# Performance work log

Measured on AMD Instinct MI355X. Metric: run time of the kernel, lower is better.

## Reference

```python
import jax, jax.numpy as jnp
import numpy as np

E = 1024
H = 16
D = E // H
S = 2048
B = 2

def setup_inputs() -> dict:
    key = jax.random.key(0)
    ks = jax.random.split(key, 5)
    x = jax.random.normal(ks[0], (B, S, E), dtype=jnp.float32)
    W_qkv = jax.random.normal(ks[1], (E, 3 * E), dtype=jnp.float32) / np.sqrt(E)
    b_qkv = jax.random.normal(ks[2], (3 * E,), dtype=jnp.float32) * 0.02
    W_out = jax.random.normal(ks[3], (E, E), dtype=jnp.float32) / np.sqrt(E)
    b_out = jax.random.normal(ks[4], (E,), dtype=jnp.float32) * 0.02
    return {"x": x, "W_qkv": W_qkv, "b_qkv": b_qkv, "W_out": W_out, "b_out": b_out}

def reference(x, W_qkv, b_qkv, W_out, b_out):
    b, s, e = x.shape
    qkv = x @ W_qkv + b_qkv                      # [B,S,3E]
    q, k, v = jnp.split(qkv, 3, axis=-1)
    # [B,S,E] -> [B,H,S,D]
    q = q.reshape(b, s, H, D).transpose(0, 2, 1, 3)
    k = k.reshape(b, s, H, D).transpose(0, 2, 1, 3)
    v = v.reshape(b, s, H, D).transpose(0, 2, 1, 3)
    scale = 1.0 / np.sqrt(D)
    att = jnp.einsum('bhqd,bhkd->bhqk', q, k) * scale
    causal = jnp.tril(jnp.ones((s, s), dtype=bool))
    att = jnp.where(causal[None, None], att, -jnp.inf)
    att = jax.nn.softmax(att, axis=-1)
    out = jnp.einsum('bhqk,bhkd->bhqd', att, v)  # [B,H,S,D]
    out = out.transpose(0, 2, 1, 3).reshape(b, s, e)
    return out @ W_out + b_out
```

## Files before the change

kernel.cpp:

```cpp
#include <hip/hip_runtime.h>

typedef unsigned short u16;
typedef __bf16  bf16x8 __attribute__((ext_vector_type(8)));
typedef float   f32x4  __attribute__((ext_vector_type(4)));
typedef unsigned int   u32x4 __attribute__((ext_vector_type(4)));
typedef unsigned short u16x4 __attribute__((ext_vector_type(4)));
typedef unsigned short u16x8 __attribute__((ext_vector_type(8)));

#define BB 2
#define HH 16
#define DD 64
#define SS 2048
#define EE 1024

#define QSCALE 0.1803368801111244f

static __device__ __forceinline__ u16 f2bf(float f) {
    unsigned int u = __float_as_uint(f);
    u += 0x7FFFu + ((u >> 16) & 1u);
    return (u16)(u >> 16);
}

union BfCast { u32x4 u; bf16x8 b; };
static __device__ __forceinline__ bf16x8 ldb8(const u16* p) {
    BfCast x; x.u = *(const u32x4*)p; return x.b;
}

static __device__ __forceinline__ void gload16(const u16* g, u16* l) {
    __builtin_amdgcn_global_load_lds(
        (const __attribute__((address_space(1))) unsigned int*)g,
        (__attribute__((address_space(3))) unsigned int*)l, 16, 0, 0);
}

#define UG (32 * 512)
static __device__ __forceinline__ int kidx(int s, int d) {
    return (((s >> 4) * 2 + (d >> 5)) * 512) + ((((d >> 3) & 3) * 16 + (s & 15)) * 8) + (d & 7);
}
static __device__ __forceinline__ int vidx(int key, int d) {
    return (((key >> 5) * 4 + (d >> 4)) * 512) + ((((key >> 3) & 3) * 16 + (d & 15)) * 8) + (key & 7);
}

__global__ __launch_bounds__(256) void prep_kernel(
    const float* __restrict__ x,    u16* __restrict__ xb,
    const float* __restrict__ Wqkv, u16* __restrict__ wqkvT,
    const float* __restrict__ Wout, u16* __restrict__ woutT)
{
    __shared__ float tile[32][33];
    const int bid = blockIdx.x;
    if (bid < 2048) {
        const int t = bid * 256 + threadIdx.x;
        const int u = t >> 6, w = t & 63;
        const int m = (u >> 5) * 16 + (w & 15);
        const int k = (u & 31) * 32 + (w >> 4) * 8;
        const float* p = x + m * 1024 + k;
        const f32x4 a = *(const f32x4*)p;
        const f32x4 b = *(const f32x4*)(p + 4);
        u16x8 o;
        o[0] = f2bf(a[0]); o[1] = f2bf(a[1]); o[2] = f2bf(a[2]); o[3] = f2bf(a[3]);
        o[4] = f2bf(b[0]); o[5] = f2bf(b[1]); o[6] = f2bf(b[2]); o[7] = f2bf(b[3]);
        *(u16x8*)&xb[u * 512 + w * 8] = o;
        return;
    }
    const float* in; u16* out; int C, tb;
    if (bid < 2048 + 3072) { in = Wqkv; out = wqkvT; C = 3072; tb = bid - 2048; }
    else                   { in = Wout; out = woutT; C = 1024; tb = bid - 5120; }
    const int tx = threadIdx.x & 31;
    const int ty = threadIdx.x >> 5;
    const int ct = C >> 5;
    const int bc = tb % ct, br = tb / ct;
    const int c0 = bc * 32, r0 = br * 32;
    #pragma unroll
    for (int i = 0; i < 4; i++)
        tile[ty + i * 8][tx] = in[(r0 + ty + i * 8) * C + c0 + tx];
    __syncthreads();
    #pragma unroll
    for (int i = 0; i < 4; i++) {
        const int n = c0 + ty + i * 8;
        out[((n >> 4) * 32 + (r0 >> 5)) * 512 + (((tx >> 3) & 3) * 16 + (n & 15)) * 8 + (tx & 7)]
            = f2bf(tile[tx][ty + i * 8]);
    }
}

__global__ __launch_bounds__(256) void gemm_qkv_kernel(
    const u16* __restrict__ Af,
    const u16* __restrict__ Bf,
    const float* __restrict__ bias,
    u16* __restrict__ Qb, u16* __restrict__ Kb, u16* __restrict__ Vb)
{
    __shared__ __align__(16) u16 Us[2][12 * 512];
    const int lane = threadIdx.x & 63;
    const int wave = threadIdx.x >> 6;
    const int nb = 3 * EE / 128;
    const int tm = blockIdx.x / nb, tn = blockIdx.x % nb;
    const int lm = lane & 15, quad = lane >> 4;

    const u16* sp[3];
    #pragma unroll
    for (int j = 0; j < 3; j++) {
        const int idx = 3 * wave + j;
        sp[j] = (idx < 4) ? (Af + (tm * 4 + idx) * UG + lane * 8)
                          : (Bf + (tn * 8 + idx - 4) * UG + lane * 8);
    }
    u16* ld0 = &Us[0][3 * wave * 512];
    u16* ld1 = &Us[1][3 * wave * 512];

    const int wy = wave >> 1, wx = wave & 1;
    f32x4 acc[2][4] = {};

    gload16(sp[0], ld0);
    gload16(sp[1], ld0 + 512);
    gload16(sp[2], ld0 + 1024);

    for (int it = 0; it < 32; ++it) {
        const int cur = it & 1;
        __syncthreads();
        if (it + 1 < 32) {
            u16* ld = cur ? ld0 : ld1;
            const int ko = (it + 1) * 512;
            gload16(sp[0] + ko, ld);
            gload16(sp[1] + ko, ld + 512);
            gload16(sp[2] + ko, ld + 1024);
        }
        bf16x8 af[2], bf[4];
        #pragma unroll
        for (int i = 0; i < 2; i++)
            af[i] = ldb8(&Us[cur][(wy * 2 + i) * 512 + lane * 8]);
        #pragma unroll
        for (int i = 0; i < 4; i++)
            bf[i] = ldb8(&Us[cur][(4 + wx * 4 + i) * 512 + lane * 8]);
        #pragma unroll
        for (int mi = 0; mi < 2; mi++)
            #pragma unroll
            for (int ni = 0; ni < 4; ni++)
                acc[mi][ni] = __builtin_amdgcn_mfma_f32_16x16x32_bf16(af[mi], bf[ni], acc[mi][ni], 0, 0, 0);
    }

    const int gm0 = tm * 64 + wy * 32;
    const int gn0 = tn * 128 + wx * 64;
    #pragma unroll
    for (int ni = 0; ni < 4; ni++) {
        const int n = gn0 + ni * 16 + lm;
        const float bv = bias[n];
        const int which = n >> 10;
        const int e = n & 1023;
        const int h = e >> 6, d = e & 63;
        #pragma unroll
        for (int mi = 0; mi < 2; mi++) {
            if (which == 2) {
                const int m0 = gm0 + mi * 16 + quad * 4;
                const int b = m0 >> 11, key0 = m0 & 2047;
                u16x4 pk;
                #pragma unroll
                for (int r = 0; r < 4; r++) pk[r] = f2bf(acc[mi][ni][r] + bv);
                *(u16x4*)&Vb[(b * HH + h) * 131072 + vidx(key0, d)] = pk;
            } else if (which == 1) {
                #pragma unroll
                for (int r = 0; r < 4; r++) {
                    const int m = gm0 + mi * 16 + quad * 4 + r;
                    const int b = m >> 11, s = m & 2047;
                    Kb[(b * HH + h) * 131072 + kidx(s, d)] = f2bf(acc[mi][ni][r] + bv);
                }
            } else {
                #pragma unroll
                for (int r = 0; r < 4; r++) {
                    const int m = gm0 + mi * 16 + quad * 4 + r;
                    const int b = m >> 11, s = m & 2047;
                    Qb[((b * HH + h) * SS + s) * DD + d] = f2bf((acc[mi][ni][r] + bv) * QSCALE);
                }
            }
        }
    }
}

__global__ __launch_bounds__(256) void attn_kernel(
    const u16* __restrict__ Qb, const u16* __restrict__ Kb,
    const u16* __restrict__ Vb, u16* __restrict__ Ob)
{
    __shared__ __align__(16) u16 Ks[2][4096];
    __shared__ __align__(16) u16 Vs[2][4096];
    __shared__ __align__(16) u16 Plds[4 * 16 * 72];
    const int tid = threadIdx.x;
    const int lane = tid & 63, wave = tid >> 6;
    const int lm = lane & 15, quad = lane >> 4;
    const int bh = blockIdx.x & 31;
    const int qt = (SS / 64 - 1) - (blockIdx.x >> 5);
    const int q0 = qt * 64;
    const int qrow = q0 + wave * 16;
    const int b = bh >> 4, h = bh & 15;

    const u16* qbase = Qb + (bh * SS + qrow) * DD;
    const bf16x8 qf0 = ldb8(qbase + lm * DD + quad * 8);
    const bf16x8 qf1 = ldb8(qbase + lm * DD + 32 + quad * 8);

    const u16* ktile = Kb + bh * 131072;
    const u16* vtile = Vb + bh * 131072;
    u16* Pw = Plds + wave * (16 * 72);

    BfCast oc; oc.u = (u32x4){0x3F803F80u, 0x3F803F80u, 0x3F803F80u, 0x3F803F80u};
    const bf16x8 ones = oc.b;

    f32x4 oacc[4] = {};
    f32x4 lacc = {0.f, 0.f, 0.f, 0.f};

    const int ktmax = qt + 1;
    {
        const u16* kg = ktile + wave * 1024 + lane * 8;
        const u16* vg = vtile + wave * 1024 + lane * 8;
        gload16(kg,       &Ks[0][wave * 1024]);
        gload16(kg + 512, &Ks[0][wave * 1024 + 512]);
        gload16(vg,       &Vs[0][wave * 1024]);
        gload16(vg + 512, &Vs[0][wave * 1024 + 512]);
    }
    for (int kt = 0; kt < ktmax; ++kt) {
        const int cur = kt & 1;
        const int k0 = kt * 64;
        __syncthreads();
        if (kt + 1 < ktmax) {
            const u16* kg = ktile + (kt + 1) * 4096 + wave * 1024 + lane * 8;
            const u16* vg = vtile + (kt + 1) * 4096 + wave * 1024 + lane * 8;
            gload16(kg,       &Ks[cur ^ 1][wave * 1024]);
            gload16(kg + 512, &Ks[cur ^ 1][wave * 1024 + 512]);
            gload16(vg,       &Vs[cur ^ 1][wave * 1024]);
            gload16(vg + 512, &Vs[cur ^ 1][wave * 1024 + 512]);
        }

        f32x4 s[4];
        #pragma unroll
        for (int g = 0; g < 4; g++) {
            f32x4 z = {0.f, 0.f, 0.f, 0.f};
            z    = __builtin_amdgcn_mfma_f32_16x16x32_bf16(ldb8(&Ks[cur][(g * 2) * 512 + lane * 8]), qf0, z, 0, 0, 0);
            s[g] = __builtin_amdgcn_mfma_f32_16x16x32_bf16(ldb8(&Ks[cur][(g * 2 + 1) * 512 + lane * 8]), qf1, z, 0, 0, 0);
        }
        if (k0 + 63 > qrow) {
            const int lim = qrow + lm - k0 - quad * 4;
            #pragma unroll
            for (int g = 0; g < 4; g++)
                #pragma unroll
                for (int r = 0; r < 4; r++)
                    if (g * 16 + r > lim) s[g][r] = -INFINITY;
        }
        #pragma unroll
        for (int g = 0; g < 4; g++) {
            u16x4 pk;
            #pragma unroll
            for (int r = 0; r < 4; r++) pk[r] = f2bf(__builtin_amdgcn_exp2f(s[g][r]));
            *(u16x4*)&Pw[lm * 72 + g * 16 + quad * 4] = pk;
        }
        const bf16x8 pf0 = ldb8(&Pw[lm * 72 + quad * 8]);
        const bf16x8 pf1 = ldb8(&Pw[lm * 72 + 32 + quad * 8]);
        lacc = __builtin_amdgcn_mfma_f32_16x16x32_bf16(ones, pf0, lacc, 0, 0, 0);
        lacc = __builtin_amdgcn_mfma_f32_16x16x32_bf16(ones, pf1, lacc, 0, 0, 0);
        #pragma unroll
        for (int dg = 0; dg < 4; dg++) {
            oacc[dg] = __builtin_amdgcn_mfma_f32_16x16x32_bf16(ldb8(&Vs[cur][dg * 512 + lane * 8]), pf0, oacc[dg], 0, 0, 0);
            oacc[dg] = __builtin_amdgcn_mfma_f32_16x16x32_bf16(ldb8(&Vs[cur][(4 + dg) * 512 + lane * 8]), pf1, oacc[dg], 0, 0, 0);
        }
    }
    const float inv = 1.0f / lacc[0];
    u16* ob = Ob + (((b * SS + qrow) >> 4) * 32 + h * 2) * 512;
    #pragma unroll
    for (int dg = 0; dg < 4; dg++) {
        u16x4 pk;
        #pragma unroll
        for (int r = 0; r < 4; r++) pk[r] = f2bf(oacc[dg][r] * inv);
        *(u16x4*)&ob[(dg >> 1) * 512 + (((dg * 2 + (quad >> 1)) & 3) * 16 + lm) * 8 + (quad & 1) * 4] = pk;
    }
}

__global__ __launch_bounds__(256) void gemm_out_kernel(
    const u16* __restrict__ Af,
    const u16* __restrict__ Bf,
    const float* __restrict__ bias,
    float* __restrict__ Out)
{
    __shared__ __align__(16) u16 Us[2][8 * 512];
    const int lane = threadIdx.x & 63;
    const int wave = threadIdx.x >> 6;
    const int nb = EE / 64;
    const int tm = blockIdx.x / nb, tn = blockIdx.x % nb;
    const int lm = lane & 15, quad = lane >> 4;

    const u16* sp[2];
    #pragma unroll
    for (int j = 0; j < 2; j++) {
        const int idx = 2 * wave + j;
        sp[j] = (idx < 4) ? (Af + (tm * 4 + idx) * UG + lane * 8)
                          : (Bf + (tn * 4 + idx - 4) * UG + lane * 8);
    }
    u16* ld0 = &Us[0][2 * wave * 512];
    u16* ld1 = &Us[1][2 * wave * 512];

    const int wy = wave >> 1, wx = wave & 1;
    f32x4 acc[2][2] = {};

    gload16(sp[0], ld0);
    gload16(sp[1], ld0 + 512);

    for (int it = 0; it < 32; ++it) {
        const int cur = it & 1;
        __syncthreads();
        if (it + 1 < 32) {
            u16* ld = cur ? ld0 : ld1;
            const int ko = (it + 1) * 512;
            gload16(sp[0] + ko, ld);
            gload16(sp[1] + ko, ld + 512);
        }
        bf16x8 af[2], bf[2];
        #pragma unroll
        for (int i = 0; i < 2; i++) {
            af[i] = ldb8(&Us[cur][(wy * 2 + i) * 512 + lane * 8]);
            bf[i] = ldb8(&Us[cur][(4 + wx * 2 + i) * 512 + lane * 8]);
        }
        #pragma unroll
        for (int mi = 0; mi < 2; mi++)
            #pragma unroll
            for (int ni = 0; ni < 2; ni++)
                acc[mi][ni] = __builtin_amdgcn_mfma_f32_16x16x32_bf16(af[mi], bf[ni], acc[mi][ni], 0, 0, 0);
    }

    const int gm0 = tm * 64 + wy * 32;
    const int gn0 = tn * 64 + wx * 32;
    #pragma unroll
    for (int ni = 0; ni < 2; ni++) {
        const int n = gn0 + ni * 16 + lm;
        const float bv = bias[n];
        #pragma unroll
        for (int mi = 0; mi < 2; mi++)
            #pragma unroll
            for (int r = 0; r < 4; r++)
                Out[(gm0 + mi * 16 + quad * 4 + r) * EE + n] = acc[mi][ni][r] + bv;
    }
}

extern "C" void kernel_launch(void* const* d_in, const int* in_sizes, int n_in,
                              void* d_out, int out_size, void* d_ws, size_t ws_size,
                              hipStream_t stream)
{
    const float* x     = (const float*)d_in[0];
    const float* Wqkv  = (const float*)d_in[1];
    const float* bqkv  = (const float*)d_in[2];
    const float* Wout  = (const float*)d_in[3];
    const float* bout  = (const float*)d_in[4];
    float* out = (float*)d_out;

    char* ws = (char*)d_ws;
    u16* xb    = (u16*)(ws + 0);
    u16* wqkvT = (u16*)(ws + 8388608);
    u16* woutT = (u16*)(ws + 14680064);
    u16* Qb    = (u16*)(ws + 16777216);
    u16* Kb    = (u16*)(ws + 25165824);
    u16* Vb    = (u16*)(ws + 33554432);
    u16* Ob    = (u16*)(ws + 41943040);
    if (ws_size < 50331648) return;

    prep_kernel<<<2048 + 3072 + 1024, 256, 0, stream>>>(x, xb, Wqkv, wqkvT, Wout, woutT);
    gemm_qkv_kernel<<<(BB * SS / 64) * (3 * EE / 128), 256, 0, stream>>>(xb, wqkvT, bqkv, Qb, Kb, Vb);
    attn_kernel<<<BB * HH * (SS / 64), 256, 0, stream>>>(Qb, Kb, Vb, Ob);
    gemm_out_kernel<<<(BB * SS / 64) * (EE / 64), 256, 0, stream>>>(Ob, woutT, bout, out);
}
```

Measured before the change: 173.9 us.

## Enlarge GEMM tiles and load A fragments directly into registers

Both GEMMs now use larger output tiles: QKV goes from 64x128 to 128x128 and the output projection from 64x64 to 64x128. Only the shared B tile is staged in LDS, and each wave loads its A fragments straight from global memory into registers with software double buffering. The aim is more reuse per loaded byte, less LDS traffic and fewer blocks. In exchange there are more accumulator registers and fewer blocks in flight, so latency hiding may suffer.

```diff
diff --git a/kernel.cpp b/kernel.cpp
--- a/kernel.cpp
+++ b/kernel.cpp
@@ -81,61 +81,77 @@
     }
 }
 
-__global__ __launch_bounds__(256) void gemm_qkv_kernel(
+__global__ __launch_bounds__(256, 3) void gemm_qkv_kernel(
     const u16* __restrict__ Af,
     const u16* __restrict__ Bf,
     const float* __restrict__ bias,
     u16* __restrict__ Qb, u16* __restrict__ Kb, u16* __restrict__ Vb)
 {
-    __shared__ __align__(16) u16 Us[2][12 * 512];
+    __shared__ __align__(16) u16 Bs[2][8 * 512];
     const int lane = threadIdx.x & 63;
     const int wave = threadIdx.x >> 6;
     const int nb = 3 * EE / 128;
     const int tm = blockIdx.x / nb, tn = blockIdx.x % nb;
     const int lm = lane & 15, quad = lane >> 4;
-
-    const u16* sp[3];
-    #pragma unroll
-    for (int j = 0; j < 3; j++) {
-        const int idx = 3 * wave + j;
-        sp[j] = (idx < 4) ? (Af + (tm * 4 + idx) * UG + lane * 8)
-                          : (Bf + (tn * 8 + idx - 4) * UG + lane * 8);
-    }
-    u16* ld0 = &Us[0][3 * wave * 512];
-    u16* ld1 = &Us[1][3 * wave * 512];
-
     const int wy = wave >> 1, wx = wave & 1;
-    f32x4 acc[2][4] = {};
-
-    gload16(sp[0], ld0);
-    gload16(sp[1], ld0 + 512);
-    gload16(sp[2], ld0 + 1024);
-
-    for (int it = 0; it < 32; ++it) {
-        const int cur = it & 1;
+
+    const u16* bg = Bf + (tn * 8 + 2 * wave) * UG + lane * 8;
+    u16* bl0 = &Bs[0][2 * wave * 512];
+    u16* bl1 = &Bs[1][2 * wave * 512];
+    const u16* ag[4];
+    #pragma unroll
+    for (int i = 0; i < 4; i++)
+        ag[i] = Af + (tm * 8 + wy * 4 + i) * UG + lane * 8;
+
+    f32x4 acc[4][4] = {};
+    bf16x8 a0[4], a1[4];
+
+    gload16(bg,      bl0);
+    gload16(bg + UG, bl0 + 512);
+    #pragma unroll
+    for (int i = 0; i < 4; i++) a0[i] = ldb8(ag[i]);
+
+    #pragma unroll 1
+    for (int it = 0; it < 32; it += 2) {
         __syncthreads();
         if (it + 1 < 32) {
-            u16* ld = cur ? ld0 : ld1;
-            const int ko = (it + 1) * 512;
-            gload16(sp[0] + ko, ld);
-            gload16(sp[1] + ko, ld + 512);
-            gload16(sp[2] + ko, ld + 1024);
-        }
-        bf16x8 af[2], bf[4];
-        #pragma unroll
-        for (int i = 0; i < 2; i++)
-            af[i] = ldb8(&Us[cur][(wy * 2 + i) * 512 + lane * 8]);
-        #pragma unroll
-        for (int i = 0; i < 4; i++)
-            bf[i] = ldb8(&Us[cur][(4 + wx * 4 + i) * 512 + lane * 8]);
-        #pragma unroll
-        for (int mi = 0; mi < 2; mi++)
-            #pragma unroll
-            for (int ni = 0; ni < 4; ni++)
-                acc[mi][ni] = __builtin_amdgcn_mfma_f32_16x16x32_bf16(af[mi], bf[ni], acc[mi][ni], 0, 0, 0);
-    }
-
-    const int gm0 = tm * 64 + wy * 32;
+            gload16(bg + (it + 1) * 512,      bl1);
+            gload16(bg + UG + (it + 1) * 512, bl1 + 512);
+            #pragma unroll
+            for (int i = 0; i < 4; i++) a1[i] = ldb8(ag[i] + (it + 1) * 512);
+        }
+        {
+            bf16x8 bf[4];
+            #pragma unroll
+            for (int i = 0; i < 4; i++)
+                bf[i] = ldb8(&Bs[0][(wx * 4 + i) * 512 + lane * 8]);
+            #pragma unroll
+            for (int mi = 0; mi < 4; mi++)
+                #pragma unroll
+                for (int ni = 0; ni < 4; ni++)
+                    acc[mi][ni] = __builtin_amdgcn_mfma_f32_16x16x32_bf16(a0[mi], bf[ni], acc[mi][ni], 0, 0, 0);
+        }
+        __syncthreads();
+        if (it + 2 < 32) {
+            gload16(bg + (it + 2) * 512,      bl0);
+            gload16(bg + UG + (it + 2) * 512, bl0 + 512);
+            #pragma unroll
+            for (int i = 0; i < 4; i++) a0[i] = ldb8(ag[i] + (it + 2) * 512);
+        }
+        {
+            bf16x8 bf[4];
+            #pragma unroll
+            for (int i = 0; i < 4; i++)
+                bf[i] = ldb8(&Bs[1][(wx * 4 + i) * 512 + lane * 8]);
+            #pragma unroll
+            for (int mi = 0; mi < 4; mi++)
+                #pragma unroll
+                for (int ni = 0; ni < 4; ni++)
+                    acc[mi][ni] = __builtin_amdgcn_mfma_f32_16x16x32_bf16(a1[mi], bf[ni], acc[mi][ni], 0, 0, 0);
+        }
+    }
+
+    const int gm0 = tm * 128 + wy * 64;
     const int gn0 = tn * 128 + wx * 64;
     #pragma unroll
     for (int ni = 0; ni < 4; ni++) {
@@ -145,7 +161,7 @@
         const int e = n & 1023;
         const int h = e >> 6, d = e & 63;
         #pragma unroll
-        for (int mi = 0; mi < 2; mi++) {
+        for (int mi = 0; mi < 4; mi++) {
             if (which == 2) {
                 const int m0 = gm0 + mi * 16 + quad * 4;
                 const int b = m0 >> 11, key0 = m0 & 2047;
@@ -273,55 +289,74 @@
     const float* __restrict__ bias,
     float* __restrict__ Out)
 {
-    __shared__ __align__(16) u16 Us[2][8 * 512];
+    __shared__ __align__(16) u16 Bs[2][8 * 512];
     const int lane = threadIdx.x & 63;
     const int wave = threadIdx.x >> 6;
-    const int nb = EE / 64;
+    const int nb = EE / 128;
     const int tm = blockIdx.x / nb, tn = blockIdx.x % nb;
     const int lm = lane & 15, quad = lane >> 4;
-
-    const u16* sp[2];
-    #pragma unroll
-    for (int j = 0; j < 2; j++) {
-        const int idx = 2 * wave + j;
-        sp[j] = (idx < 4) ? (Af + (tm * 4 + idx) * UG + lane * 8)
-                          : (Bf + (tn * 4 + idx - 4) * UG + lane * 8);
-    }
-    u16* ld0 = &Us[0][2 * wave * 512];
-    u16* ld1 = &Us[1][2 * wave * 512];
-
     const int wy = wave >> 1, wx = wave & 1;
-    f32x4 acc[2][2] = {};
-
-    gload16(sp[0], ld0);
-    gload16(sp[1], ld0 + 512);
-
-    for (int it = 0; it < 32; ++it) {
-        const int cur = it & 1;
+
+    const u16* bg = Bf + (tn * 8 + 2 * wave) * UG + lane * 8;
+    u16* bl0 = &Bs[0][2 * wave * 512];
+    u16* bl1 = &Bs[1][2 * wave * 512];
+    const u16* ag[2];
+    #pragma unroll
+    for (int i = 0; i < 2; i++)
+        ag[i] = Af + (tm * 4 + wy * 2 + i) * UG + lane * 8;
+
+    f32x4 acc[2][4] = {};
+    bf16x8 a0[2], a1[2];
+
+    gload16(bg,      bl0);
+    gload16(bg + UG, bl0 + 512);
+    #pragma unroll
+    for (int i = 0; i < 2; i++) a0[i] = ldb8(ag[i]);
+
+    #pragma unroll 1
+    for (int it = 0; it < 32; it += 2) {
         __syncthreads();
         if (it + 1 < 32) {
-            u16* ld = cur ? ld0 : ld1;
-            const int ko = (it + 1) * 512;
-            gload16(sp[0] + ko, ld);
-            gload16(sp[1] + ko, ld + 512);
-        }
-        bf16x8 af[2], bf[2];
-        #pragma unroll
-        for (int i = 0; i < 2; i++) {
-            af[i] = ldb8(&Us[cur][(wy * 2 + i) * 512 + lane * 8]);
-            bf[i] = ldb8(&Us[cur][(4 + wx * 2 + i) * 512 + lane * 8]);
-        }
-        #pragma unroll
-        for (int mi = 0; mi < 2; mi++)
-            #pragma unroll
-            for (int ni = 0; ni < 2; ni++)
-                acc[mi][ni] = __builtin_amdgcn_mfma_f32_16x16x32_bf16(af[mi], bf[ni], acc[mi][ni], 0, 0, 0);
+            gload16(bg + (it + 1) * 512,      bl1);
+            gload16(bg + UG + (it + 1) * 512, bl1 + 512);
+            #pragma unroll
+            for (int i = 0; i < 2; i++) a1[i] = ldb8(ag[i] + (it + 1) * 512);
+        }
+        {
+            bf16x8 bf[4];
+            #pragma unroll
+            for (int i = 0; i < 4; i++)
+                bf[i] = ldb8(&Bs[0][(wx * 4 + i) * 512 + lane * 8]);
+            #pragma unroll
+            for (int mi = 0; mi < 2; mi++)
+                #pragma unroll
+                for (int ni = 0; ni < 4; ni++)
+                    acc[mi][ni] = __builtin_amdgcn_mfma_f32_16x16x32_bf16(a0[mi], bf[ni], acc[mi][ni], 0, 0, 0);
+        }
+        __syncthreads();
+        if (it + 2 < 32) {
+            gload16(bg + (it + 2) * 512,      bl0);
+            gload16(bg + UG + (it + 2) * 512, bl0 + 512);
+            #pragma unroll
+            for (int i = 0; i < 2; i++) a0[i] = ldb8(ag[i] + (it + 2) * 512);
+        }
+        {
+            bf16x8 bf[4];
+            #pragma unroll
+            for (int i = 0; i < 4; i++)
+                bf[i] = ldb8(&Bs[1][(wx * 4 + i) * 512 + lane * 8]);
+            #pragma unroll
+            for (int mi = 0; mi < 2; mi++)
+                #pragma unroll
+                for (int ni = 0; ni < 4; ni++)
+                    acc[mi][ni] = __builtin_amdgcn_mfma_f32_16x16x32_bf16(a1[mi], bf[ni], acc[mi][ni], 0, 0, 0);
+        }
     }
 
     const int gm0 = tm * 64 + wy * 32;
-    const int gn0 = tn * 64 + wx * 32;
-    #pragma unroll
-    for (int ni = 0; ni < 2; ni++) {
+    const int gn0 = tn * 128 + wx * 64;
+    #pragma unroll
+    for (int ni = 0; ni < 4; ni++) {
         const int n = gn0 + ni * 16 + lm;
         const float bv = bias[n];
         #pragma unroll
@@ -354,7 +389,7 @@
     if (ws_size < 50331648) return;
 
     prep_kernel<<<2048 + 3072 + 1024, 256, 0, stream>>>(x, xb, Wqkv, wqkvT, Wout, woutT);
-    gemm_qkv_kernel<<<(BB * SS / 64) * (3 * EE / 128), 256, 0, stream>>>(xb, wqkvT, bqkv, Qb, Kb, Vb);
+    gemm_qkv_kernel<<<(BB * SS / 128) * (3 * EE / 128), 256, 0, stream>>>(xb, wqkvT, bqkv, Qb, Kb, Vb);
     attn_kernel<<<BB * HH * (SS / 64), 256, 0, stream>>>(Qb, Kb, Vb, Ob);
-    gemm_out_kernel<<<(BB * SS / 64) * (EE / 64), 256, 0, stream>>>(Ob, woutT, bout, out);
-}
+    gemm_out_kernel<<<(BB * SS / 64) * (EE / 128), 256, 0, stream>>>(Ob, woutT, bout, out);
+}
```

Measured after the change: 174.8 us. Within noise of the previous version (+0.5%).
